# Optimization experiments

Hardware: AMD Instinct MI355X
Metric: run time of the kernel (lower is better)

The kernel has to match this reference:

```python
import jax, jax.numpy as jnp
import numpy as np


def setup_inputs() -> dict:
    key0 = jax.random.key(0)
    ks = jax.random.split(key0, 6)
    b, q, k = 4, 256, 1024
    emb_q = emb_k = emb_v = 256
    h = 128
    query = jax.random.normal(ks[0], (b, q, emb_q), dtype=jnp.float32)
    key = jax.random.normal(ks[1], (b, k, emb_k), dtype=jnp.float32)
    value = jax.random.normal(ks[2], (b, k, emb_v), dtype=jnp.float32)
    # linear_uniform_ style init: U(-1/sqrt(in), 1/sqrt(in))
    wq = jax.random.uniform(ks[3], (emb_q, h), minval=-1.0, maxval=1.0) / np.sqrt(emb_q)
    wk = jax.random.uniform(ks[4], (emb_k, h), minval=-1.0, maxval=1.0) / np.sqrt(emb_k)
    wv = jax.random.uniform(ks[5], (h,), minval=-1.0, maxval=1.0) / np.sqrt(h)
    return {"query": query, "key": key, "value": value,
            "weight_query": wq.astype(jnp.float32),
            "weight_key": wk.astype(jnp.float32),
            "weight_value": wv.astype(jnp.float32)}


def reference(query, key, value, weight_query, weight_key, weight_value):
    # Additive (Bahdanau) attention.
    Hq = jnp.einsum('bqe,eh->bqh', query, weight_query)   # (b, q, h)
    Hk = jnp.einsum('bke,eh->bkh', key, weight_key)       # (b, k, h)
    # broadcast-add + tanh: (b, q, k, h)
    H = jnp.tanh(Hq[:, :, None, :] + Hk[:, None, :, :])
    z = jnp.einsum('bqkh,h->bqk', H, weight_value)        # scores (b, q, k)
    a = jax.nn.softmax(z, axis=-1)                        # (b, q, k)
    out = jnp.einsum('bqk,bkv->bqv', a, value)            # (b, q, emb_v)
    return out, a
```

## Files before the change

kernel.cpp:

```cpp
#include <hip/hip_runtime.h>


#define L2E 1.4426950408889634f

__global__ __launch_bounds__(256) void aa_proj_kernel(
    const float* __restrict__ query, const float* __restrict__ key,
    const float* __restrict__ wq, const float* __restrict__ wk,
    float* __restrict__ Eq, float* __restrict__ Ek)
{
    __shared__ float rows_s[16 * 256];
    __shared__ float w_s[64 * 128];
    const int i = blockIdx.x;
    const int t = threadIdx.x;

    const float* src;
    const float* W;
    float* dst;
    if (i < 64) {
        const int r0 = i * 16;
        src = query + r0 * 256; W = wq; dst = Eq + r0 * 128;
    } else {
        const int r0 = (i - 64) * 16;
        src = key + r0 * 256; W = wk; dst = Ek + r0 * 128;
    }

#pragma unroll
    for (int j = 0; j < 4; ++j) {
        const int f = t * 4 + j * 1024;
        *(float4*)&rows_s[f] = *(const float4*)&src[f];
    }

    const int rgr = t >> 5;
    const int hg = t & 31;
    const int ri0 = rgr * 2;
    const int h0 = hg * 4;

    float acc0[4] = {0.f, 0.f, 0.f, 0.f};
    float acc1[4] = {0.f, 0.f, 0.f, 0.f};

    for (int ec = 0; ec < 256; ec += 64) {
        __syncthreads();
#pragma unroll
        for (int j = 0; j < 8; ++j) {
            const int f = t * 4 + j * 1024;
            *(float4*)&w_s[f] = *(const float4*)&W[ec * 128 + f];
        }
        __syncthreads();

        for (int e = 0; e < 64; e += 4) {
            float a0[4], a1[4];
            *(float4*)a0 = *(const float4*)&rows_s[ri0 * 256 + ec + e];
            *(float4*)a1 = *(const float4*)&rows_s[(ri0 + 1) * 256 + ec + e];
#pragma unroll
            for (int j = 0; j < 4; ++j) {
                float w[4];
                *(float4*)w = *(const float4*)&w_s[(e + j) * 128 + h0];
#pragma unroll
                for (int c = 0; c < 4; ++c) {
                    acc0[c] = fmaf(a0[j], w[c], acc0[c]);
                    acc1[c] = fmaf(a1[j], w[c], acc1[c]);
                }
            }
        }
    }

    float o0[4], o1[4];
#pragma unroll
    for (int c = 0; c < 4; ++c) {
        o0[c] = __builtin_amdgcn_exp2f(acc0[c] * (2.0f * L2E));
        o1[c] = __builtin_amdgcn_exp2f(acc1[c] * (2.0f * L2E));
    }
    *(float4*)&dst[ri0 * 128 + h0] = *(float4*)o0;
    *(float4*)&dst[(ri0 + 1) * 128 + h0] = *(float4*)o1;
}

__global__ __launch_bounds__(256) void aa_score_kernel(
    const float* __restrict__ Eq, const float* __restrict__ Ek,
    const float* __restrict__ wv, float* __restrict__ z)
{
    __shared__ float eq_s[16 * 128];
    __shared__ float ek_s[128 * 132];
    __shared__ float wv_s[128];

    const int bid = blockIdx.x;
    const int b  = bid >> 7;
    const int qt = (bid >> 3) & 15;
    const int kt = bid & 7;
    const int q0g = b * 256 + qt * 16;
    const int k0g = b * 1024 + kt * 128;
    const int t = threadIdx.x;

    const float* eqsrc = Eq + (size_t)q0g * 128;
#pragma unroll
    for (int j = 0; j < 2; ++j) {
        const int f = t * 4 + j * 1024;
        *(float4*)&eq_s[f] = *(const float4*)&eqsrc[f];
    }
    const float* eksrc = Ek + (size_t)k0g * 128;
#pragma unroll
    for (int j = 0; j < 16; ++j) {
        const int f = t * 4 + j * 1024;
        const int ki = f >> 7;
        const int h = f & 127;
        *(float4*)&ek_s[ki * 132 + h] = *(const float4*)&eksrc[f];
    }
    if (t < 128) wv_s[t] = wv[t];
    __syncthreads();

    const int qp = t >> 6;
    const int kp = t & 63;
    const float* eq0 = eq_s + (qp * 4) * 128;
    const float* eka = ek_s + kp * 132;
    const float* ekb = eka + 64 * 132;

    float acc[4][2] = {};

    auto quad = [](const float* x, const float* y, const float* w, float& acc) {
        const float A = fmaf(x[0], y[0], 1.0f);
        const float B = fmaf(x[1], y[1], 1.0f);
        const float C = fmaf(x[2], y[2], 1.0f);
        const float D = fmaf(x[3], y[3], 1.0f);
        const float AB = A * B;
        const float CD = C * D;
        const float n01 = fmaf(w[1], A, w[0] * B);
        const float n23 = fmaf(w[3], C, w[2] * D);
        const float num = fmaf(n01, CD, n23 * AB);
        acc = fmaf(num, __builtin_amdgcn_rcpf(AB * CD), acc);
    };

#pragma unroll 4
    for (int h = 0; h < 128; h += 4) {
        float y0[4], y1[4], w4[4];
        *(float4*)y0 = *(const float4*)(eka + h);
        *(float4*)y1 = *(const float4*)(ekb + h);
        *(float4*)w4 = *(const float4*)(wv_s + h);
#pragma unroll
        for (int i = 0; i < 4; ++i) {
            float x[4];
            *(float4*)x = *(const float4*)(eq0 + i * 128 + h);
            quad(x, y0, w4, acc[i][0]);
            quad(x, y1, w4, acc[i][1]);
        }
    }

    const int kl = kt * 128 + kp;
#pragma unroll
    for (int i = 0; i < 4; ++i) {
        float* zr = z + (size_t)(q0g + qp * 4 + i) * 1024 + kl;
        zr[0]  = -2.0f * acc[i][0];
        zr[64] = -2.0f * acc[i][1];
    }
}

__global__ __launch_bounds__(256) void aa_softmax_kernel(
    const float* __restrict__ z, float* __restrict__ a)
{
    const int row = blockIdx.x;
    const int t = threadIdx.x;
    const float* zr = z + (size_t)row * 1024;

    float x[4];
    *(float4*)x = *(const float4*)&zr[t * 4];

    float m = fmaxf(fmaxf(x[0], x[1]), fmaxf(x[2], x[3]));
#pragma unroll
    for (int off = 32; off; off >>= 1) m = fmaxf(m, __shfl_xor(m, off));

    __shared__ float redm[4];
    __shared__ float reds[4];
    const int wid = t >> 6;
    if ((t & 63) == 0) redm[wid] = m;
    __syncthreads();
    m = fmaxf(fmaxf(redm[0], redm[1]), fmaxf(redm[2], redm[3]));

    float e[4];
    float s = 0.f;
#pragma unroll
    for (int j = 0; j < 4; ++j) {
        e[j] = __builtin_amdgcn_exp2f((x[j] - m) * L2E);
        s += e[j];
    }
#pragma unroll
    for (int off = 32; off; off >>= 1) s += __shfl_xor(s, off);
    if ((t & 63) == 0) reds[wid] = s;
    __syncthreads();
    s = reds[0] + reds[1] + reds[2] + reds[3];

    const float inv = __builtin_amdgcn_rcpf(s);
    float o[4];
#pragma unroll
    for (int j = 0; j < 4; ++j) o[j] = e[j] * inv;
    *(float4*)&a[(size_t)row * 1024 + t * 4] = *(float4*)o;
}

__global__ __launch_bounds__(512) void aa_pv_partial_kernel(
    const float* __restrict__ a, const float* __restrict__ value,
    float* __restrict__ part)
{
    __shared__ float a_s[16][256];
    __shared__ float red_s[8][4096];
    const int bid = blockIdx.x;
    const int b  = bid >> 6;
    const int qt = (bid >> 2) & 15;
    const int kt = bid & 3;
    const int t = threadIdx.x;

#pragma unroll
    for (int j = 0; j < 2; ++j) {
        const int f = t * 4 + j * 2048;
        const int qs = f >> 8;
        const int k0 = f & 255;
        const float* arow = a + (size_t)(b * 256 + qt * 16 + qs) * 1024 + kt * 256;
        *(float4*)&a_s[qs][k0] = *(const float4*)&arow[k0];
    }
    __syncthreads();

    const int w = t >> 6;
    const int lane = t & 63;
    const int v0 = lane * 4;
    const float* vp = value + (size_t)b * 262144
                    + (size_t)(kt * 256 + w * 32) * 256 + v0;

    float acc[16][4] = {};

#pragma unroll 2
    for (int k4 = 0; k4 < 8; ++k4) {
        float vv[4][4];
#pragma unroll
        for (int r = 0; r < 4; ++r)
            *(float4*)vv[r] = *(const float4*)(vp + (size_t)(k4 * 4 + r) * 256);
#pragma unroll
        for (int q = 0; q < 16; ++q) {
            float aq[4];
            *(float4*)aq = *(const float4*)&a_s[q][w * 32 + k4 * 4];
#pragma unroll
            for (int r = 0; r < 4; ++r)
#pragma unroll
                for (int c = 0; c < 4; ++c)
                    acc[q][c] = fmaf(aq[r], vv[r][c], acc[q][c]);
        }
    }

    float* rs = &red_s[w][v0];
#pragma unroll
    for (int q = 0; q < 16; ++q)
        *(float4*)(rs + q * 256) = *(float4*)acc[q];
    __syncthreads();

    float* po = part + (size_t)bid * 4096;
#pragma unroll
    for (int c = 0; c < 2; ++c) {
        const int i = c * 2048 + t * 4;
        float s[4];
        *(float4*)s = *(const float4*)&red_s[0][i];
#pragma unroll
        for (int ww = 1; ww < 8; ++ww) {
            float x[4];
            *(float4*)x = *(const float4*)&red_s[ww][i];
            s[0] += x[0]; s[1] += x[1]; s[2] += x[2]; s[3] += x[3];
        }
        *(float4*)(po + i) = *(float4*)s;
    }
}

__global__ __launch_bounds__(256) void aa_pv_reduce_kernel(
    const float* __restrict__ part, float* __restrict__ out)
{
    const int idx = blockIdx.x * 256 + threadIdx.x;
    const int o = idx * 4;
    const int row = o >> 8;
    const int v = o & 255;
    const int b = row >> 8;
    const int q = row & 255;
    const int qt = q >> 4;
    const int qr = q & 15;
    const float* p = part + (size_t)((b * 16 + qt) * 4) * 4096 + qr * 256 + v;

    float s[4] = {0.f, 0.f, 0.f, 0.f};
#pragma unroll
    for (int kt = 0; kt < 4; ++kt) {
        float x[4];
        *(float4*)x = *(const float4*)(p + (size_t)kt * 4096);
        s[0] += x[0]; s[1] += x[1]; s[2] += x[2]; s[3] += x[3];
    }
    *(float4*)&out[o] = *(float4*)s;
}

extern "C" void kernel_launch(void* const* d_in, const int* in_sizes, int n_in,
                              void* d_out, int out_size, void* d_ws, size_t ws_size,
                              hipStream_t stream)
{
    const float* query = (const float*)d_in[0];
    const float* key   = (const float*)d_in[1];
    const float* value = (const float*)d_in[2];
    const float* wq    = (const float*)d_in[3];
    const float* wk    = (const float*)d_in[4];
    const float* wv    = (const float*)d_in[5];

    float* out   = (float*)d_out;
    float* a_out = out + 4 * 256 * 256;

    float* ws = (float*)d_ws;
    float* Eq   = ws;
    float* Ek   = ws + 131072;
    float* z    = ws + 131072 + 524288;
    float* part = ws + 131072 + 524288 + 1048576;

    aa_proj_kernel<<<320, 256, 0, stream>>>(query, key, wq, wk, Eq, Ek);
    aa_score_kernel<<<512, 256, 0, stream>>>(Eq, Ek, wv, z);
    aa_softmax_kernel<<<1024, 256, 0, stream>>>(z, a_out);
    aa_pv_partial_kernel<<<256, 512, 0, stream>>>(a_out, value, part);
    aa_pv_reduce_kernel<<<256, 256, 0, stream>>>(part, out);
}
```

Before: 49.16 us.

## Fuse softmax into score and PV kernels via per-tile max/sum stats

Removes the standalone softmax kernel. The score kernel now writes per-tile row max and exp-sum statistics alongside z. The PV partial kernel merges these online-softmax style, normalizes z into probabilities on load, and writes the attention output. This drops one launch and one full read and write of the score matrix, at the cost of extra shuffle reductions in the score kernel and redundant stats merging across PV blocks.

```diff
diff --git a/kernel.cpp b/kernel.cpp
--- a/kernel.cpp
+++ b/kernel.cpp
@@ -76,7 +76,8 @@
 
 __global__ __launch_bounds__(256) void aa_score_kernel(
     const float* __restrict__ Eq, const float* __restrict__ Ek,
-    const float* __restrict__ wv, float* __restrict__ z)
+    const float* __restrict__ wv, float* __restrict__ z,
+    float* __restrict__ stats)
 {
     __shared__ float eq_s[16 * 128];
     __shared__ float ek_s[128 * 132];
@@ -146,72 +147,77 @@
     const int kl = kt * 128 + kp;
 #pragma unroll
     for (int i = 0; i < 4; ++i) {
+        const float z0 = -2.0f * acc[i][0];
+        const float z1 = -2.0f * acc[i][1];
         float* zr = z + (size_t)(q0g + qp * 4 + i) * 1024 + kl;
-        zr[0]  = -2.0f * acc[i][0];
-        zr[64] = -2.0f * acc[i][1];
-    }
-}
-
-__global__ __launch_bounds__(256) void aa_softmax_kernel(
-    const float* __restrict__ z, float* __restrict__ a)
-{
-    const int row = blockIdx.x;
-    const int t = threadIdx.x;
-    const float* zr = z + (size_t)row * 1024;
-
-    float x[4];
-    *(float4*)x = *(const float4*)&zr[t * 4];
-
-    float m = fmaxf(fmaxf(x[0], x[1]), fmaxf(x[2], x[3]));
-#pragma unroll
-    for (int off = 32; off; off >>= 1) m = fmaxf(m, __shfl_xor(m, off));
-
-    __shared__ float redm[4];
-    __shared__ float reds[4];
-    const int wid = t >> 6;
-    if ((t & 63) == 0) redm[wid] = m;
-    __syncthreads();
-    m = fmaxf(fmaxf(redm[0], redm[1]), fmaxf(redm[2], redm[3]));
-
-    float e[4];
-    float s = 0.f;
-#pragma unroll
-    for (int j = 0; j < 4; ++j) {
-        e[j] = __builtin_amdgcn_exp2f((x[j] - m) * L2E);
-        s += e[j];
-    }
-#pragma unroll
-    for (int off = 32; off; off >>= 1) s += __shfl_xor(s, off);
-    if ((t & 63) == 0) reds[wid] = s;
-    __syncthreads();
-    s = reds[0] + reds[1] + reds[2] + reds[3];
-
-    const float inv = __builtin_amdgcn_rcpf(s);
-    float o[4];
-#pragma unroll
-    for (int j = 0; j < 4; ++j) o[j] = e[j] * inv;
-    *(float4*)&a[(size_t)row * 1024 + t * 4] = *(float4*)o;
+        zr[0]  = z0;
+        zr[64] = z1;
+
+        float mx = fmaxf(z0, z1);
+#pragma unroll
+        for (int off = 32; off; off >>= 1) mx = fmaxf(mx, __shfl_xor(mx, off));
+        float e = __builtin_amdgcn_exp2f((z0 - mx) * L2E)
+                + __builtin_amdgcn_exp2f((z1 - mx) * L2E);
+#pragma unroll
+        for (int off = 32; off; off >>= 1) e += __shfl_xor(e, off);
+        if (kp == 0) {
+            float* sp = stats + (size_t)(bid * 16 + qp * 4 + i) * 2;
+            sp[0] = mx;
+            sp[1] = e;
+        }
+    }
 }
 
 __global__ __launch_bounds__(512) void aa_pv_partial_kernel(
-    const float* __restrict__ a, const float* __restrict__ value,
-    float* __restrict__ part)
+    const float* __restrict__ z, const float* __restrict__ stats,
+    const float* __restrict__ value,
+    float* __restrict__ a, float* __restrict__ part)
 {
     __shared__ float a_s[16][256];
     __shared__ float red_s[8][4096];
+    __shared__ float ms_s[16];
+    __shared__ float is_s[16];
     const int bid = blockIdx.x;
     const int b  = bid >> 6;
     const int qt = (bid >> 2) & 15;
     const int kt = bid & 3;
     const int t = threadIdx.x;
 
+    if (t < 16) {
+        const float* st = stats + (size_t)(b * 128 + qt * 8) * 32;
+        float mloc[8], sloc[8];
+#pragma unroll
+        for (int k8 = 0; k8 < 8; ++k8) {
+            mloc[k8] = st[(k8 * 16 + t) * 2];
+            sloc[k8] = st[(k8 * 16 + t) * 2 + 1];
+        }
+        float m = mloc[0];
+#pragma unroll
+        for (int k8 = 1; k8 < 8; ++k8) m = fmaxf(m, mloc[k8]);
+        float s = 0.f;
+#pragma unroll
+        for (int k8 = 0; k8 < 8; ++k8)
+            s = fmaf(sloc[k8], __builtin_amdgcn_exp2f((mloc[k8] - m) * L2E), s);
+        ms_s[t] = m;
+        is_s[t] = __builtin_amdgcn_rcpf(s);
+    }
+    __syncthreads();
+
 #pragma unroll
     for (int j = 0; j < 2; ++j) {
         const int f = t * 4 + j * 2048;
         const int qs = f >> 8;
         const int k0 = f & 255;
-        const float* arow = a + (size_t)(b * 256 + qt * 16 + qs) * 1024 + kt * 256;
-        *(float4*)&a_s[qs][k0] = *(const float4*)&arow[k0];
+        const size_t roff = (size_t)(b * 256 + qt * 16 + qs) * 1024 + kt * 256 + k0;
+        float x[4], o[4];
+        *(float4*)x = *(const float4*)&z[roff];
+        const float m = ms_s[qs];
+        const float inv = is_s[qs];
+#pragma unroll
+        for (int c = 0; c < 4; ++c)
+            o[c] = __builtin_amdgcn_exp2f((x[c] - m) * L2E) * inv;
+        *(float4*)&a_s[qs][k0] = *(float4*)o;
+        *(float4*)&a[roff] = *(float4*)o;
     }
     __syncthreads();
 
@@ -301,14 +307,14 @@
     float* a_out = out + 4 * 256 * 256;
 
     float* ws = (float*)d_ws;
-    float* Eq   = ws;
-    float* Ek   = ws + 131072;
-    float* z    = ws + 131072 + 524288;
-    float* part = ws + 131072 + 524288 + 1048576;
+    float* Eq    = ws;
+    float* Ek    = ws + 131072;
+    float* z     = ws + 131072 + 524288;
+    float* part  = ws + 131072 + 524288 + 1048576;
+    float* stats = ws + 131072 + 524288 + 2097152;
 
     aa_proj_kernel<<<320, 256, 0, stream>>>(query, key, wq, wk, Eq, Ek);
-    aa_score_kernel<<<512, 256, 0, stream>>>(Eq, Ek, wv, z);
-    aa_softmax_kernel<<<1024, 256, 0, stream>>>(z, a_out);
-    aa_pv_partial_kernel<<<256, 512, 0, stream>>>(a_out, value, part);
+    aa_score_kernel<<<512, 256, 0, stream>>>(Eq, Ek, wv, z, stats);
+    aa_pv_partial_kernel<<<256, 512, 0, stream>>>(z, stats, value, a_out, part);
     aa_pv_reduce_kernel<<<256, 256, 0, stream>>>(part, out);
 }
```

Measured after the change: 48.69 us. About the same (-1.0%).
